# Kernel optimization log

Hardware: AMD Instinct MI355X
Metric: run time of the kernel (lower is better)

## Reference

```python
import jax, jax.numpy as jnp
import numpy as np

EPS = 1e-5

def conv_act_norm(x, W, b, a, g, be):
    """1x1 Conv2d -> PReLU -> LayerNormalization4D (normalize over channel dim).
    x: [B,C,T,F]; W: [O,C]; b,g,be: [O]; a: PReLU scalar."""
    y = jnp.einsum('bctf,oc->botf', x, W) + b[None, :, None, None]
    y = jnp.where(y >= 0, y, a * y)
    mu = y.mean(axis=1, keepdims=True)
    var = y.var(axis=1, keepdims=True)
    y = (y - mu) * jax.lax.rsqrt(var + EPS)
    return y * g[None, :, None, None] + be[None, :, None, None]


def setup_inputs() -> dict:
    key = jax.random.key(0)
    B, C, T, F = 2, 64, 2048, 64
    H, HC = 4, 4            # n_head, hid_chan
    VC = C // H             # value channels per head = 16
    ks = jax.random.split(key, 16)
    s = 0.05
    inp = {
        'x': jax.random.normal(ks[0], (B, C, T, F), jnp.float32),
        # per-head Q projections (stacked along leading head axis)
        'Wq': jax.random.normal(ks[1], (H, HC, C), jnp.float32) * s,
        'bq': jnp.zeros((H, HC), jnp.float32),
        'aq': jnp.full((H,), 0.25, jnp.float32),
        'gq': jnp.ones((H, HC), jnp.float32),
        'betaq': jnp.zeros((H, HC), jnp.float32),
        # per-head K projections
        'Wk': jax.random.normal(ks[2], (H, HC, C), jnp.float32) * s,
        'bk': jnp.zeros((H, HC), jnp.float32),
        'ak': jnp.full((H,), 0.25, jnp.float32),
        'gk': jnp.ones((H, HC), jnp.float32),
        'betak': jnp.zeros((H, HC), jnp.float32),
        # per-head V projections
        'Wv': jax.random.normal(ks[3], (H, VC, C), jnp.float32) * s,
        'bv': jnp.zeros((H, VC), jnp.float32),
        'av': jnp.full((H,), 0.25, jnp.float32),
        'gv': jnp.ones((H, VC), jnp.float32),
        'betav': jnp.zeros((H, VC), jnp.float32),
        # output concat projection
        'Wp': jax.random.normal(ks[4], (C, C), jnp.float32) * s,
        'bp': jnp.zeros((C,), jnp.float32),
        'ap': jnp.asarray(0.25, jnp.float32),
        'gp': jnp.ones((C,), jnp.float32),
        'betap': jnp.zeros((C,), jnp.float32),
    }
    return inp


def reference(x, Wq, bq, aq, gq, betaq, Wk, bk, ak, gk, betak,
              Wv, bv, av, gv, betav, Wp, bp, ap, gp, betap):
    H = Wq.shape[0]
    B, C, T, F = x.shape
    per_head = jax.vmap(conv_act_norm, in_axes=(None, 0, 0, 0, 0, 0))
    Q = per_head(x, Wq, bq, aq, gq, betaq)      # [H,B,HC,T,F]
    K = per_head(x, Wk, bk, ak, gk, betak)      # [H,B,HC,T,F]
    V = per_head(x, Wv, bv, av, gv, betav)      # [H,B,VC,T,F]
    # flatten: sequence over time, embedding = channels*freq
    Qf = Q.transpose(0, 1, 3, 2, 4).reshape(H, B, T, -1)   # [H,B,T,HC*F]
    Kf = K.transpose(0, 1, 3, 2, 4).reshape(H, B, T, -1)
    Vt = V.transpose(0, 1, 3, 2, 4)                          # [H,B,T,VC,F]
    Vf = Vt.reshape(H, B, T, -1)                             # [H,B,T,VC*F]
    d = Qf.shape[-1]
    scale = jnp.asarray(1.0 / np.sqrt(d), x.dtype)
    attn = jnp.einsum('hbtd,hbsd->hbts', Qf, Kf) * scale    # [H,B,T,T]
    attn = jax.nn.softmax(attn, axis=-1)
    O = jnp.einsum('hbts,hbsd->hbtd', attn, Vf).reshape(Vt.shape)  # [H,B,T,VC,F]
    # back to [B, H*VC, T, F] with head-major channel ordering (matches torch view)
    O = O.transpose(1, 0, 3, 2, 4).reshape(B, C, T, F)
    out = conv_act_norm(O, Wp, bp, ap, gp, betap)
    return out + x
```

## Files before the change

kernel.cpp:

```cpp
#include <hip/hip_runtime.h>
#include <stdint.h>

typedef unsigned short ushort_t;
typedef unsigned int u32;
typedef short bf16x8 __attribute__((ext_vector_type(8)));
typedef float f32x4 __attribute__((ext_vector_type(4)));

#define MFMA16(a, b, c) __builtin_amdgcn_mfma_f32_16x16x32_bf16((a), (b), (c), 0, 0, 0)

__device__ __forceinline__ ushort_t f2bf(float f) {
  union { float f; u32 u; } v; v.f = f;
  return (ushort_t)((v.u + 0x7FFFu + ((v.u >> 16) & 1u)) >> 16);
}
__device__ __forceinline__ float bf2f(ushort_t h) {
  union { u32 u; float f; } v; v.u = ((u32)h) << 16;
  return v.f;
}

__global__ __launch_bounds__(512, 4) void k_proj_qkv(
    const float* __restrict__ x,
    const float* __restrict__ Wq, const float* __restrict__ bq, const float* __restrict__ aq,
    const float* __restrict__ gq, const float* __restrict__ beq,
    const float* __restrict__ Wk, const float* __restrict__ bk, const float* __restrict__ ak,
    const float* __restrict__ gk, const float* __restrict__ bek,
    const float* __restrict__ Wv, const float* __restrict__ bv, const float* __restrict__ av,
    const float* __restrict__ gv, const float* __restrict__ bev,
    ushort_t* __restrict__ Qp, ushort_t* __restrict__ Kp, ushort_t* __restrict__ Vp)
{
  __shared__ ushort_t lds_q[16 * 136];
  __shared__ ushort_t lds_k[16 * 136];
  __shared__ ushort_t lds_v[512 * 24];

  const int tid = threadIdx.x;
  const int fi = tid & 31, ti = tid >> 5;
  const int lane = tid & 63, wid = tid >> 6;
  const int bid = blockIdx.x;
  const int tt = bid & 127;
  const int fh = (bid >> 7) & 1;
  const int b  = bid >> 8;
  const int t = tt * 16 + ti;
  const int f = fh * 32 + fi;

  float xr[64];
  {
    const float* xp = x + ((size_t)b * 64 * 2048 + t) * 64 + f;
#pragma unroll
    for (int c = 0; c < 64; ++c) xr[c] = xp[(size_t)c * (2048 * 64)];
  }

#pragma unroll 1
  for (int h = 0; h < 4; ++h) {
    const int hb = h * 2 + b;
    float qa[4], ka[4], va[16];
#pragma unroll
    for (int j = 0; j < 4; ++j) { qa[j] = bq[h * 4 + j]; ka[j] = bk[h * 4 + j]; }
#pragma unroll
    for (int j = 0; j < 16; ++j) va[j] = bv[h * 16 + j];
    for (int c = 0; c < 64; ++c) {
      float xv = xr[c];
#pragma unroll
      for (int j = 0; j < 4; ++j) qa[j] += Wq[(h * 4 + j) * 64 + c] * xv;
#pragma unroll
      for (int j = 0; j < 4; ++j) ka[j] += Wk[(h * 4 + j) * 64 + c] * xv;
#pragma unroll
      for (int j = 0; j < 16; ++j) va[j] += Wv[(h * 16 + j) * 64 + c] * xv;
    }
    {
      float aa = aq[h], mu = 0.f;
#pragma unroll
      for (int j = 0; j < 4; ++j) { float u = qa[j]; u = u >= 0.f ? u : aa * u; qa[j] = u; mu += u; }
      mu *= 0.25f;
      float var = 0.f;
#pragma unroll
      for (int j = 0; j < 4; ++j) { float d = qa[j] - mu; var += d * d; }
      float is = rsqrtf(var * 0.25f + 1e-5f);
#pragma unroll
      for (int j = 0; j < 4; ++j) {
        float v = ((qa[j] - mu) * is * gq[h * 4 + j] + beq[h * 4 + j]) * 0.0625f;
        lds_q[ti * 136 + j * 32 + fi] = f2bf(v);
      }
    }
    {
      float aa = ak[h], mu = 0.f;
#pragma unroll
      for (int j = 0; j < 4; ++j) { float u = ka[j]; u = u >= 0.f ? u : aa * u; ka[j] = u; mu += u; }
      mu *= 0.25f;
      float var = 0.f;
#pragma unroll
      for (int j = 0; j < 4; ++j) { float d = ka[j] - mu; var += d * d; }
      float is = rsqrtf(var * 0.25f + 1e-5f);
#pragma unroll
      for (int j = 0; j < 4; ++j) {
        float v = (ka[j] - mu) * is * gk[h * 4 + j] + bek[h * 4 + j];
        lds_k[ti * 136 + j * 32 + fi] = f2bf(v);
      }
    }
    {
      float aa = av[h], mu = 0.f;
#pragma unroll
      for (int j = 0; j < 16; ++j) { float u = va[j]; u = u >= 0.f ? u : aa * u; va[j] = u; mu += u; }
      mu *= 0.0625f;
      float var = 0.f;
#pragma unroll
      for (int j = 0; j < 16; ++j) { float d = va[j] - mu; var += d * d; }
      float is = rsqrtf(var * 0.0625f + 1e-5f);
#pragma unroll
      for (int vc = 0; vc < 16; ++vc) {
        float v = (va[vc] - mu) * is * gv[h * 16 + vc] + bev[h * 16 + vc];
        lds_v[(vc * 32 + fi) * 24 + ti] = f2bf(v);
      }
    }
    __syncthreads();

    {
      int j = wid & 3;
      const ushort_t* src = (wid < 4) ? lds_q : lds_k;
      uint4 v = *(const uint4*)&src[(lane & 15) * 136 + j * 32 + ((lane >> 4) << 3)];
      size_t base = ((((size_t)hb * 128 + tt) * 8) + (2 * j + fh)) << 9;
      ushort_t* dst = (wid < 4) ? Qp : Kp;
      *(uint4*)(dst + base + ((size_t)lane << 3)) = v;
    }
    {
      const int halfsel = tt & 1;
      const bool act = (lane >> 5) == halfsel;
#pragma unroll
      for (int i = 0; i < 4; ++i) {
        int gl = wid * 4 + i;
        int vc = gl >> 1, u = gl & 1;
        int row = vc * 32 + u * 16 + (lane & 15);
        uint4 v = *(const uint4*)&lds_v[row * 24 + (((lane >> 4) & 1) << 3)];
        int g = vc * 4 + fh * 2 + u;
        size_t base = (((size_t)hb * 64 + (tt >> 1)) * 64 + g) << 9;
        if (act) *(uint4*)(Vp + base + ((size_t)lane << 3)) = v;
      }
    }
    __syncthreads();
  }
}

__global__ __launch_bounds__(512, 4) void k_attn(
    const ushort_t* __restrict__ Qp, const ushort_t* __restrict__ Kp,
    const ushort_t* __restrict__ Vp, ushort_t* __restrict__ O)
{
  extern __shared__ char smem[];
  ushort_t* Kbuf = (ushort_t*)smem;
  ushort_t* Qlds = (ushort_t*)(smem + 32768);
  ushort_t* Plds = (ushort_t*)(smem + 65536);
  float* pmax  = (float*)(smem + 69632);
  float* psum  = (float*)(smem + 70144);
  float* rsrow = (float*)(smem + 70656);
  float* lrow  = (float*)(smem + 70912);
  int*   skipf = (int*)(smem + 71168);

  const int lane = threadIdx.x & 63;
  const int wid  = threadIdx.x >> 6;
  const int qblk = wid >> 1;
  const int tsh  = wid & 1;
  const int hb = blockIdx.x & 7;
  const int r2 = blockIdx.x >> 3;
  const int dvh = r2 & 1;
  const int qtile = r2 >> 1;
  const int tb4 = (lane >> 4) << 2;
  const int rowbase = qblk * 16 + tb4;

  {
    const ushort_t* qsrc = Qp + (((size_t)(hb * 128 + qtile * 4)) << 12) + ((size_t)lane << 3);
#pragma unroll
    for (int i = 0; i < 4; ++i) {
      int c = wid * 4 + i;
      *(uint4*)(Qlds + ((size_t)c << 9) + ((size_t)lane << 3)) = *(const uint4*)(qsrc + ((size_t)c << 9));
    }
    const ushort_t* ksrc = Kp + (((size_t)(hb * 128)) << 12) + ((size_t)lane << 3);
#pragma unroll
    for (int i = 0; i < 2; ++i) {
      int c = wid * 2 + i;
      *(uint4*)(Kbuf + ((size_t)c << 9) + ((size_t)lane << 3)) = *(const uint4*)(ksrc + ((size_t)c << 9));
    }
  }
  __syncthreads();

  f32x4 acc[16];
#pragma unroll
  for (int i = 0; i < 16; ++i) acc[i] = (f32x4){0.f, 0.f, 0.f, 0.f};
  float m_run[4], l_run[4];
#pragma unroll
  for (int r = 0; r < 4; ++r) { m_run[r] = -1e30f; l_run[r] = 0.f; }

  for (int s = 0; s < 64; ++s) {
    uint4 kst0, kst1;
    {
      int sn = (s + 1) & 63;
      const ushort_t* ksrc = Kp + (((size_t)(hb * 128 + 2 * sn)) << 12) + ((size_t)lane << 3);
      kst0 = *(const uint4*)(ksrc + ((size_t)(wid * 2 + 0) << 9));
      kst1 = *(const uint4*)(ksrc + ((size_t)(wid * 2 + 1) << 9));
    }

    const ushort_t* kb = Kbuf + (((size_t)(s & 1)) << 13);
    f32x4 sacc = (f32x4){0.f, 0.f, 0.f, 0.f};
    __builtin_amdgcn_s_setprio(1);
#pragma unroll
    for (int kk = 0; kk < 8; ++kk) {
      bf16x8 qf = *(const bf16x8*)(Qlds + (((size_t)(qblk * 8 + kk)) << 9) + ((size_t)lane << 3));
      bf16x8 kf = *(const bf16x8*)(kb + (((size_t)(tsh * 8 + kk)) << 9) + ((size_t)lane << 3));
      sacc = MFMA16(qf, kf, sacc);
    }
    __builtin_amdgcn_s_setprio(0);
    float rm[4];
#pragma unroll
    for (int r = 0; r < 4; ++r) rm[r] = sacc[r];
#pragma unroll
    for (int m = 1; m <= 8; m <<= 1) {
#pragma unroll
      for (int r = 0; r < 4; ++r) rm[r] = fmaxf(rm[r], __shfl_xor(rm[r], m));
    }
    if ((lane & 15) == 0)
      *(f32x4*)&pmax[tsh * 64 + rowbase] = (f32x4){rm[0], rm[1], rm[2], rm[3]};
    __syncthreads();

    f32x4 pm0 = *(const f32x4*)&pmax[rowbase];
    f32x4 pm1 = *(const f32x4*)&pmax[64 + rowbase];
    float mn[4], rs[4], pv[4];
    int okl = 1;
#pragma unroll
    for (int r = 0; r < 4; ++r) {
      mn[r] = fmaxf(m_run[r], fmaxf(pm0[r], pm1[r]));
      okl &= (mn[r] - m_run[r] <= 8.0f) ? 1 : 0;
    }
    const int ok = __all(okl);
    if (!ok) {
#pragma unroll
      for (int r = 0; r < 4; ++r) { rs[r] = __expf(m_run[r] - mn[r]); m_run[r] = mn[r]; }
    } else {
#pragma unroll
      for (int r = 0; r < 4; ++r) rs[r] = 1.0f;
    }
#pragma unroll
    for (int r = 0; r < 4; ++r) pv[r] = __expf(sacc[r] - m_run[r]);
    float ps[4];
#pragma unroll
    for (int r = 0; r < 4; ++r) ps[r] = pv[r];
#pragma unroll
    for (int m = 1; m <= 8; m <<= 1) {
#pragma unroll
      for (int r = 0; r < 4; ++r) ps[r] += __shfl_xor(ps[r], m);
    }
    if ((lane & 15) == 0) {
      *(f32x4*)&psum[tsh * 64 + rowbase] = (f32x4){ps[0], ps[1], ps[2], ps[3]};
      if (tsh == 0)
        *(f32x4*)&rsrow[rowbase] = (f32x4){rs[0], rs[1], rs[2], rs[3]};
    }
    if (tsh == 0 && lane == 0) skipf[qblk] = ok;
    {
      int ts = tsh * 16 + (lane & 15);
      int cs = (ts >> 3) << 4;
      int jj = ts & 7;
#pragma unroll
      for (int r = 0; r < 4; ++r) {
        int tgt = (tb4 + r) | cs;
        Plds[(((size_t)qblk) << 9) + (tgt << 3) + jj] = f2bf(pv[r]);
      }
    }
    __syncthreads();

    {
      ushort_t* kdst = Kbuf + (((size_t)((s + 1) & 1)) << 13) + ((size_t)lane << 3);
      *(uint4*)(kdst + ((size_t)(wid * 2 + 0) << 9)) = kst0;
      *(uint4*)(kdst + ((size_t)(wid * 2 + 1) << 9)) = kst1;
    }

    {
      {
        f32x4 s0 = *(const f32x4*)&psum[rowbase];
        f32x4 s1 = *(const f32x4*)&psum[64 + rowbase];
#pragma unroll
        for (int r = 0; r < 4; ++r) l_run[r] = l_run[r] * rs[r] + s0[r] + s1[r];
      }
      const int dvt0 = dvh * 32 + wid * 4;
      const ushort_t* vh0 = Vp + ((((size_t)hb * 64 + s) * 64 + dvt0) << 9) + ((size_t)lane << 3);
#pragma unroll
      for (int ip = 0; ip < 2; ++ip) {
        bf16x8 vh_a = *(const bf16x8*)(vh0 + ((size_t)(ip * 2 + 0) << 9));
        bf16x8 vh_b = *(const bf16x8*)(vh0 + ((size_t)(ip * 2 + 1) << 9));
        __builtin_amdgcn_s_setprio(1);
#pragma unroll
        for (int q = 0; q < 4; ++q) {
          bf16x8 pf = *(const bf16x8*)(Plds + (((size_t)q) << 9) + ((size_t)lane << 3));
          int ia = q * 4 + ip * 2 + 0;
          int ib = q * 4 + ip * 2 + 1;
          if (!skipf[q]) {
            f32x4 rq = *(const f32x4*)&rsrow[q * 16 + tb4];
#pragma unroll
            for (int r = 0; r < 4; ++r) { acc[ia][r] *= rq[r]; acc[ib][r] *= rq[r]; }
          }
          acc[ia] = MFMA16(pf, vh_a, acc[ia]);
          acc[ib] = MFMA16(pf, vh_b, acc[ib]);
        }
        __builtin_amdgcn_s_setprio(0);
      }
    }
    __syncthreads();
  }

  if (tsh == 0 && (lane & 15) == 0)
    *(f32x4*)&lrow[rowbase] = (f32x4){l_run[0], l_run[1], l_run[2], l_run[3]};
  __syncthreads();

  const int h = hb >> 1, b = hb & 1;
#pragma unroll
  for (int q = 0; q < 4; ++q) {
    f32x4 lq = *(const f32x4*)&lrow[q * 16 + tb4];
    f32x4 inv;
#pragma unroll
    for (int r = 0; r < 4; ++r) inv[r] = 1.0f / lq[r];
    int trow = qtile * 64 + q * 16 + tb4;
#pragma unroll
    for (int i = 0; i < 4; ++i) {
      int dv = dvh * 512 + wid * 64 + i * 16 + (lane & 15);
      ushort_t* op = O + (((size_t)b * 64 + h * 16 + (dv >> 6)) * 2048 + trow) * 64 + (dv & 63);
#pragma unroll
      for (int r = 0; r < 4; ++r) op[(size_t)r * 64] = f2bf(acc[q * 4 + i][r] * inv[r]);
    }
  }
}

__global__ __launch_bounds__(256) void k_outproj(
    const ushort_t* __restrict__ O, const float* __restrict__ Wp, const float* __restrict__ bp,
    const float* __restrict__ ap, const float* __restrict__ gp, const float* __restrict__ bep,
    const float* __restrict__ x, float* __restrict__ out)
{
  int tid = blockIdx.x * 256 + threadIdx.x;
  int f = tid & 63;
  int t = (tid >> 6) & 2047;
  int b = tid >> 17;

  float acc[64];
#pragma unroll
  for (int o = 0; o < 64; ++o) acc[o] = bp[o];
  const ushort_t* op_ = O + ((size_t)b * 64 * 2048 + t) * 64 + f;
  for (int c = 0; c < 64; ++c) {
    float ov = bf2f(op_[(size_t)c * (2048 * 64)]);
#pragma unroll
    for (int o = 0; o < 64; ++o) acc[o] += Wp[o * 64 + c] * ov;
  }
  float aa = ap[0];
  float mu = 0.f;
#pragma unroll
  for (int o = 0; o < 64; ++o) { float y = acc[o]; y = y >= 0.f ? y : aa * y; acc[o] = y; mu += y; }
  mu *= 0.015625f;
  float var = 0.f;
#pragma unroll
  for (int o = 0; o < 64; ++o) { float d = acc[o] - mu; var += d * d; }
  float is = rsqrtf(var * 0.015625f + 1e-5f);
  size_t base = ((size_t)b * 64 * 2048 + t) * 64 + f;
#pragma unroll
  for (int o = 0; o < 64; ++o) {
    size_t idx = base + (size_t)o * (2048 * 64);
    out[idx] = (acc[o] - mu) * is * gp[o] + bep[o] + x[idx];
  }
}

extern "C" void kernel_launch(void* const* d_in, const int* in_sizes, int n_in,
                              void* d_out, int out_size, void* d_ws, size_t ws_size,
                              hipStream_t stream) {
  (void)in_sizes; (void)n_in; (void)out_size; (void)ws_size;
  const float* x   = (const float*)d_in[0];
  const float* Wq  = (const float*)d_in[1];
  const float* bq  = (const float*)d_in[2];
  const float* aq  = (const float*)d_in[3];
  const float* gq  = (const float*)d_in[4];
  const float* beq = (const float*)d_in[5];
  const float* Wk  = (const float*)d_in[6];
  const float* bk  = (const float*)d_in[7];
  const float* ak  = (const float*)d_in[8];
  const float* gk  = (const float*)d_in[9];
  const float* bek = (const float*)d_in[10];
  const float* Wv  = (const float*)d_in[11];
  const float* bv  = (const float*)d_in[12];
  const float* av  = (const float*)d_in[13];
  const float* gv  = (const float*)d_in[14];
  const float* bev = (const float*)d_in[15];
  const float* Wp  = (const float*)d_in[16];
  const float* bp  = (const float*)d_in[17];
  const float* ap  = (const float*)d_in[18];
  const float* gp  = (const float*)d_in[19];
  const float* bep = (const float*)d_in[20];

  char* ws = (char*)d_ws;
  const size_t MB = 1024 * 1024;
  ushort_t* Qp   = (ushort_t*)(ws + 0 * MB);
  ushort_t* Kp   = (ushort_t*)(ws + 8 * MB);
  ushort_t* Vp   = (ushort_t*)(ws + 16 * MB);
  ushort_t* Obuf = (ushort_t*)(ws + 48 * MB);

  hipFuncSetAttribute((const void*)k_attn, hipFuncAttributeMaxDynamicSharedMemorySize, 71296);

  k_proj_qkv<<<512, 512, 0, stream>>>(x, Wq, bq, aq, gq, beq, Wk, bk, ak, gk, bek,
                                      Wv, bv, av, gv, bev, Qp, Kp, Vp);
  k_attn<<<512, 512, 71296, stream>>>(Qp, Kp, Vp, Obuf);
  k_outproj<<<1024, 256, 0, stream>>>(Obuf, Wp, bp, ap, gp, bep, x, (float*)d_out);
}
```

Baseline: 520.2 us.

## Write attention output in MFMA fragment layout and use MFMA in output projection

The attention kernel now stages its normalized output through LDS and writes it to global memory in a fragment-packed layout matched to the B operand of a 16x16x32 bf16 MFMA. The output projection is rewritten to load Wp once as bf16 A fragments and compute the 64x64 channel mix with MFMA instead of a scalar per-thread 64-accumulator loop. LayerNorm statistics are computed with cross-lane shuffles using a sum and sum-of-squares formulation. The projection kernel's launch-bounds occupancy hint is lowered from 4 to 2. The risks are an extra LDS pass and barrier in attention, rounding Wp to bf16, and the less stable single-pass variance.

```diff
diff --git a/kernel.cpp b/kernel.cpp
--- a/kernel.cpp
+++ b/kernel.cpp
@@ -17,7 +17,7 @@
   return v.f;
 }
 
-__global__ __launch_bounds__(512, 4) void k_proj_qkv(
+__global__ __launch_bounds__(512, 2) void k_proj_qkv(
     const float* __restrict__ x,
     const float* __restrict__ Wq, const float* __restrict__ bq, const float* __restrict__ aq,
     const float* __restrict__ gq, const float* __restrict__ beq,
@@ -140,7 +140,7 @@
 
 __global__ __launch_bounds__(512, 4) void k_attn(
     const ushort_t* __restrict__ Qp, const ushort_t* __restrict__ Kp,
-    const ushort_t* __restrict__ Vp, ushort_t* __restrict__ O)
+    const ushort_t* __restrict__ Vp, ushort_t* __restrict__ Ofrag)
 {
   extern __shared__ char smem[];
   ushort_t* Kbuf = (ushort_t*)smem;
@@ -151,6 +151,7 @@
   float* rsrow = (float*)(smem + 70656);
   float* lrow  = (float*)(smem + 70912);
   int*   skipf = (int*)(smem + 71168);
+  ushort_t* Olds = (ushort_t*)smem;
 
   const int lane = threadIdx.x & 63;
   const int wid  = threadIdx.x >> 6;
@@ -312,50 +313,108 @@
     f32x4 inv;
 #pragma unroll
     for (int r = 0; r < 4; ++r) inv[r] = 1.0f / lq[r];
-    int trow = qtile * 64 + q * 16 + tb4;
 #pragma unroll
     for (int i = 0; i < 4; ++i) {
-      int dv = dvh * 512 + wid * 64 + i * 16 + (lane & 15);
-      ushort_t* op = O + (((size_t)b * 64 + h * 16 + (dv >> 6)) * 2048 + trow) * 64 + (dv & 63);
-#pragma unroll
-      for (int r = 0; r < 4; ++r) op[(size_t)r * 64] = f2bf(acc[q * 4 + i][r] * inv[r]);
-    }
+      int fcol = i * 16 + (lane & 15);
+#pragma unroll
+      for (int r = 0; r < 4; ++r) {
+        int tl = q * 16 + tb4 + r;
+        Olds[((size_t)(tl * 64 + fcol) << 3) + wid] = f2bf(acc[q * 4 + i][r] * inv[r]);
+      }
+    }
+  }
+  __syncthreads();
+
+  const int kf = (h * 2 + dvh) >> 2;
+  const int lgrp = (h * 2 + dvh) & 3;
+  const size_t pfibase = (size_t)(b * 8192 + qtile * 256);
+#pragma unroll
+  for (int grp = 0; grp < 8; ++grp) {
+    int tl = wid * 8 + grp;
+    int fq = lane >> 4, l = lane & 15;
+    uint4 v = *(const uint4*)&Olds[(size_t)(tl * 64 + fq * 16 + l) << 3];
+    size_t pfi = pfibase + tl * 4 + fq;
+    *(uint4*)(Ofrag + ((pfi * 2 + kf) << 9) + ((size_t)(lgrp * 16 + l) << 3)) = v;
   }
 }
 
 __global__ __launch_bounds__(256) void k_outproj(
-    const ushort_t* __restrict__ O, const float* __restrict__ Wp, const float* __restrict__ bp,
+    const ushort_t* __restrict__ Ofrag, const float* __restrict__ Wp, const float* __restrict__ bp,
     const float* __restrict__ ap, const float* __restrict__ gp, const float* __restrict__ bep,
     const float* __restrict__ x, float* __restrict__ out)
 {
-  int tid = blockIdx.x * 256 + threadIdx.x;
-  int f = tid & 63;
-  int t = (tid >> 6) & 2047;
-  int b = tid >> 17;
-
-  float acc[64];
-#pragma unroll
-  for (int o = 0; o < 64; ++o) acc[o] = bp[o];
-  const ushort_t* op_ = O + ((size_t)b * 64 * 2048 + t) * 64 + f;
-  for (int c = 0; c < 64; ++c) {
-    float ov = bf2f(op_[(size_t)c * (2048 * 64)]);
-#pragma unroll
-    for (int o = 0; o < 64; ++o) acc[o] += Wp[o * 64 + c] * ov;
-  }
-  float aa = ap[0];
-  float mu = 0.f;
-#pragma unroll
-  for (int o = 0; o < 64; ++o) { float y = acc[o]; y = y >= 0.f ? y : aa * y; acc[o] = y; mu += y; }
-  mu *= 0.015625f;
-  float var = 0.f;
-#pragma unroll
-  for (int o = 0; o < 64; ++o) { float d = acc[o] - mu; var += d * d; }
-  float is = rsqrtf(var * 0.015625f + 1e-5f);
-  size_t base = ((size_t)b * 64 * 2048 + t) * 64 + f;
-#pragma unroll
-  for (int o = 0; o < 64; ++o) {
-    size_t idx = base + (size_t)o * (2048 * 64);
-    out[idx] = (acc[o] - mu) * is * gp[o] + bep[o] + x[idx];
+  const int lane = threadIdx.x & 63;
+  const int wid  = threadIdx.x >> 6;
+
+  bf16x8 a[4][2];
+#pragma unroll
+  for (int mt = 0; mt < 4; ++mt) {
+#pragma unroll
+    for (int kfr = 0; kfr < 2; ++kfr) {
+      const float* wsrc = Wp + (size_t)(mt * 16 + (lane & 15)) * 64 + kfr * 32 + ((lane >> 4) << 3);
+      float4 w0 = *(const float4*)wsrc;
+      float4 w1 = *(const float4*)(wsrc + 4);
+      bf16x8 af;
+      af[0] = (short)f2bf(w0.x); af[1] = (short)f2bf(w0.y);
+      af[2] = (short)f2bf(w0.z); af[3] = (short)f2bf(w0.w);
+      af[4] = (short)f2bf(w1.x); af[5] = (short)f2bf(w1.y);
+      af[6] = (short)f2bf(w1.z); af[7] = (short)f2bf(w1.w);
+      a[mt][kfr] = af;
+    }
+  }
+  float4 bb[4], gg[4], be_[4];
+#pragma unroll
+  for (int mt = 0; mt < 4; ++mt) {
+    int ob = mt * 16 + ((lane >> 4) << 2);
+    bb[mt] = *(const float4*)(bp + ob);
+    gg[mt] = *(const float4*)(gp + ob);
+    be_[mt] = *(const float4*)(bep + ob);
+  }
+  const float aa = ap[0];
+
+#pragma unroll 1
+  for (int pt = 0; pt < 4; ++pt) {
+    const int pfi = blockIdx.x * 16 + wid * 4 + pt;
+    const ushort_t* bsrc = Ofrag + (((size_t)pfi * 2) << 9) + ((size_t)lane << 3);
+    bf16x8 b0 = *(const bf16x8*)bsrc;
+    bf16x8 b1 = *(const bf16x8*)(bsrc + 512);
+
+    f32x4 acc[4];
+#pragma unroll
+    for (int mt = 0; mt < 4; ++mt) {
+      acc[mt] = MFMA16(a[mt][0], b0, ((f32x4){0.f, 0.f, 0.f, 0.f}));
+      acc[mt] = MFMA16(a[mt][1], b1, acc[mt]);
+    }
+    float s1 = 0.f, s2 = 0.f;
+#pragma unroll
+    for (int mt = 0; mt < 4; ++mt) {
+#pragma unroll
+      for (int j = 0; j < 4; ++j) {
+        float y = acc[mt][j] + bb[mt][j];
+        y = y >= 0.f ? y : aa * y;
+        acc[mt][j] = y;
+        s1 += y; s2 += y * y;
+      }
+    }
+    s1 += __shfl_xor(s1, 16); s1 += __shfl_xor(s1, 32);
+    s2 += __shfl_xor(s2, 16); s2 += __shfl_xor(s2, 32);
+    float mu = s1 * 0.015625f;
+    float var = s2 * 0.015625f - mu * mu;
+    float is = rsqrtf(var + 1e-5f);
+
+    const int b = pfi >> 13;
+    const int posl = (pfi & 8191) * 16 + (lane & 15);
+    const float* xbase = x + (size_t)b * 8388608 + posl;
+    float* obase = out + (size_t)b * 8388608 + posl;
+#pragma unroll
+    for (int mt = 0; mt < 4; ++mt) {
+#pragma unroll
+      for (int j = 0; j < 4; ++j) {
+        int o = mt * 16 + ((lane >> 4) << 2) + j;
+        float r = (acc[mt][j] - mu) * is * gg[mt][j] + be_[mt][j] + xbase[(size_t)o * 131072];
+        obase[(size_t)o * 131072] = r;
+      }
+    }
   }
 }
 
@@ -387,15 +446,15 @@
 
   char* ws = (char*)d_ws;
   const size_t MB = 1024 * 1024;
-  ushort_t* Qp   = (ushort_t*)(ws + 0 * MB);
-  ushort_t* Kp   = (ushort_t*)(ws + 8 * MB);
-  ushort_t* Vp   = (ushort_t*)(ws + 16 * MB);
-  ushort_t* Obuf = (ushort_t*)(ws + 48 * MB);
+  ushort_t* Qp    = (ushort_t*)(ws + 0 * MB);
+  ushort_t* Kp    = (ushort_t*)(ws + 8 * MB);
+  ushort_t* Vp    = (ushort_t*)(ws + 16 * MB);
+  ushort_t* Ofrag = (ushort_t*)(ws + 48 * MB);
 
   hipFuncSetAttribute((const void*)k_attn, hipFuncAttributeMaxDynamicSharedMemorySize, 71296);
 
   k_proj_qkv<<<512, 512, 0, stream>>>(x, Wq, bq, aq, gq, beq, Wk, bk, ak, gk, bek,
                                       Wv, bv, av, gv, bev, Qp, Kp, Vp);
-  k_attn<<<512, 512, 71296, stream>>>(Qp, Kp, Vp, Obuf);
-  k_outproj<<<1024, 256, 0, stream>>>(Obuf, Wp, bp, ap, gp, bep, x, (float*)d_out);
-}
+  k_attn<<<512, 512, 71296, stream>>>(Qp, Kp, Vp, Ofrag);
+  k_outproj<<<1024, 256, 0, stream>>>(Ofrag, Wp, bp, ap, gp, bep, x, (float*)d_out);
+}
```

Result: no change. 519.2 us (-0.2%).
